# Optimization experiments

Measured on AMD Instinct MI355X. Metric: run time of the kernel, lower is better.

Reference implementation:

```python
import jax, jax.numpy as jnp
import numpy as np

N_HEADS = 16


def _rope(q, k, freq_cos, freq_sin):
    # q,k: [B,S,H,hd]; freqs: [S, hd//2]
    B, S, H, hd = q.shape
    qr, qi = q.reshape(B, S, H, hd // 2, 2)[..., 0], q.reshape(B, S, H, hd // 2, 2)[..., 1]
    kr, ki = k.reshape(B, S, H, hd // 2, 2)[..., 0], k.reshape(B, S, H, hd // 2, 2)[..., 1]
    fc = freq_cos[None, :, None, :]  # [1,S,1,hd//2]
    fs = freq_sin[None, :, None, :]
    q_out = jnp.stack([qr * fc - qi * fs, qr * fs + qi * fc], axis=-1).reshape(B, S, H, hd)
    k_out = jnp.stack([kr * fc - ki * fs, kr * fs + ki * fc], axis=-1).reshape(B, S, H, hd)
    return q_out, k_out


def setup_inputs() -> dict:
    key = jax.random.key(0)
    ks = jax.random.split(key, 7)
    B, S, D = 2, 2048, 2048
    hd = D // N_HEADS
    scale = 1.0 / np.sqrt(D)
    return {
        "x": jax.random.normal(ks[0], (B, S, D), dtype=jnp.float32),
        "freq_cos": jnp.cos(jax.random.normal(ks[1], (S, hd // 2), dtype=jnp.float32)),
        "freq_sin": jnp.sin(jax.random.normal(ks[2], (S, hd // 2), dtype=jnp.float32)),
        "wq": jax.random.normal(ks[3], (D, D), dtype=jnp.float32) * scale,
        "wk": jax.random.normal(ks[4], (D, D), dtype=jnp.float32) * scale,
        "wv": jax.random.normal(ks[5], (D, D), dtype=jnp.float32) * scale,
        "wo": jax.random.normal(ks[6], (D, D), dtype=jnp.float32) * scale,
    }


def reference(x, freq_cos, freq_sin, wq, wk, wv, wo):
    B, S, D = x.shape
    H = N_HEADS
    hd = D // H
    # torch nn.Linear(weight [out,in]): y = x @ W^T
    q = (x @ wq.T).reshape(B, S, H, hd)
    k = (x @ wk.T).reshape(B, S, H, hd)
    v = (x @ wv.T).reshape(B, S, H, hd)
    q, k = _rope(q, k, freq_cos, freq_sin)
    # [B,H,S,hd]
    q = q.transpose(0, 2, 1, 3)
    k = k.transpose(0, 2, 1, 3)
    v = v.transpose(0, 2, 1, 3)
    scores = jnp.einsum("bhqd,bhkd->bhqk", q, k) / jnp.sqrt(jnp.float32(hd))
    causal = jnp.triu(jnp.full((S, S), -jnp.inf, dtype=scores.dtype), k=1)
    scores = scores + causal[None, None, :, :]
    probs = jax.nn.softmax(scores, axis=-1)
    out = jnp.einsum("bhqk,bhkd->bhqd", probs, v)
    out = out.transpose(0, 2, 1, 3).reshape(B, S, D)
    return out @ wo.T
```

## Files before the change

kernel.cpp:

```cpp
#include <hip/hip_runtime.h>
#include <hip/hip_bf16.h>
#include <stdint.h>

typedef unsigned short u16;
typedef unsigned int   u32;

typedef __attribute__((ext_vector_type(8))) short bf16x8;
typedef __attribute__((ext_vector_type(4))) float f32x4;
typedef __attribute__((ext_vector_type(4))) float f4;
typedef __attribute__((ext_vector_type(4))) u16   u16x4;

#define GLOBAL_AS __attribute__((address_space(1)))
#define LDS_AS    __attribute__((address_space(3)))

#define QSCALE (0.088388347648318447f * 1.4426950408889634f)

__device__ __forceinline__ void gload_lds16(const void* gsrc, void* ldst) {
    __builtin_amdgcn_global_load_lds((GLOBAL_AS const u32*)gsrc,
                                     (LDS_AS u32*)ldst, 16, 0, 0);
}

__device__ __forceinline__ float b2f(u16 u) {
    union { u32 i; float f; } x; x.i = ((u32)u) << 16; return x.f;
}
__device__ __forceinline__ u16 f2b(float f) {
    u32 u = __builtin_bit_cast(u32, f);
    u = (u + 0x7fff + ((u >> 16) & 1)) >> 16;
    return (u16)u;
}
__device__ __forceinline__ u16 f2b_tr(float f) {
    return (u16)(__builtin_bit_cast(u32, f) >> 16);
}

__global__ __launch_bounds__(256)
void f2bf_all(const float* __restrict__ x,  const float* __restrict__ wq,
              const float* __restrict__ wk, const float* __restrict__ wv,
              const float* __restrict__ wo, u16* __restrict__ out,
              int md4, int dd4, int n4) {
    int i = blockIdx.x * blockDim.x + threadIdx.x;
    if (i >= n4) return;
    const float* src; int off;
    if (i < md4) { src = x; off = i; }
    else {
        int j = i - md4;
        int k = j / dd4;
        off = j - k * dd4;
        src = (k == 0) ? wq : (k == 1) ? wk : (k == 2) ? wv : wo;
    }
    f4 v = ((const f4*)src)[off];
    u16x4 o;
    o[0] = f2b(v[0]); o[1] = f2b(v[1]); o[2] = f2b(v[2]); o[3] = f2b(v[3]);
    ((u16x4*)out)[i] = o;
}

#define BARR() do { asm volatile("" ::: "memory"); \
                    __builtin_amdgcn_s_barrier();  \
                    asm volatile("" ::: "memory"); } while (0)

template<int OUT_MODE>
__global__ __launch_bounds__(512, 2)
void gemm8(const u16* __restrict__ A, const u16* __restrict__ B,
           void* __restrict__ Cptr, int M, int N, int Kdim,
           const float* __restrict__ fc, const float* __restrict__ fs) {
    __shared__ char lds[131072];
    const int t = threadIdx.x, l = t & 63, w = t >> 6;
    const int g = l >> 4, r16 = l & 15;
    const int wm = w >> 2, wn = w & 3;

    const int nwg = gridDim.x * gridDim.y;
    const int id  = blockIdx.y * gridDim.x + blockIdx.x;
    const int swz = (id & 7) * (nwg >> 3) + (id >> 3);
    const int bx  = swz % gridDim.x, by = swz / gridDim.x;
    const int m0 = by * 256, n0 = bx * 256;

    f32x4 acc[8][4];
#pragma unroll
    for (int i = 0; i < 8; i++)
#pragma unroll
        for (int j = 0; j < 4; j++) acc[i][j] = (f32x4){0.f, 0.f, 0.f, 0.f};

    const int sw  = (r16 & 7) << 4;
    const int cK0 = (g * 16) ^ sw;
    const int cK1 = (64 + g * 16) ^ sw;

    bf16x8 afA[4][2], bfA[2][2], bfB[2][2];

    auto stgA = [&](int d, int r, int kt) {
#pragma unroll
        for (int i = 0; i < 2; i++) {
            const int o  = (i * 8 + w) * 1024 + l * 16;
            const int rr = o >> 7;
            const int cb = (o & 127) ^ ((rr & 7) << 4);
            const int gr = ((rr >> 6) << 7) + r * 64 + (rr & 63);
            gload_lds16(A + (size_t)(m0 + gr) * Kdim + kt * 64 + (cb >> 1),
                        lds + d * 65536 + r * 16384 + (i * 8 + w) * 1024);
        }
    };
    auto stgB = [&](int d, int r, int kt) {
#pragma unroll
        for (int i = 0; i < 2; i++) {
            const int o  = (i * 8 + w) * 1024 + l * 16;
            const int rr = o >> 7;
            const int cb = (o & 127) ^ ((rr & 7) << 4);
            const int gc = ((rr >> 5) << 6) + r * 32 + (rr & 31);
            gload_lds16(B + (size_t)(n0 + gc) * Kdim + kt * 64 + (cb >> 1),
                        lds + d * 65536 + 32768 + r * 16384 + (i * 8 + w) * 1024);
        }
    };
    auto rdA = [&](int d, int qm) {
#pragma unroll
        for (int mi = 0; mi < 4; mi++) {
            const char* p = lds + d * 65536 + qm * 16384
                            + (wm * 64 + mi * 16 + r16) * 128;
            afA[mi][0] = *(const bf16x8*)(p + cK0);
            afA[mi][1] = *(const bf16x8*)(p + cK1);
        }
    };
    auto rdB = [&](bf16x8 (&dst)[2][2], int d, int qn) {
#pragma unroll
        for (int ni = 0; ni < 2; ni++) {
            const char* p = lds + d * 65536 + 32768 + qn * 16384
                            + (wn * 32 + ni * 16 + r16) * 128;
            dst[ni][0] = *(const bf16x8*)(p + cK0);
            dst[ni][1] = *(const bf16x8*)(p + cK1);
        }
    };
    auto mm = [&](int qm, int qn, bf16x8 (&bf)[2][2]) {
        __builtin_amdgcn_s_setprio(1);
#pragma unroll
        for (int kk = 0; kk < 2; kk++)
#pragma unroll
            for (int mi = 0; mi < 4; mi++)
#pragma unroll
                for (int ni = 0; ni < 2; ni++)
                    acc[qm * 4 + mi][qn * 2 + ni] =
                        __builtin_amdgcn_mfma_f32_16x16x32_bf16(
                            afA[mi][kk], bf[ni][kk],
                            acc[qm * 4 + mi][qn * 2 + ni], 0, 0, 0);
        __builtin_amdgcn_s_setprio(0);
    };

    const int nk = Kdim >> 6;

    stgA(0, 0, 0); stgB(0, 1, 0); stgB(0, 0, 0); stgA(0, 1, 0);
    stgA(1, 0, 1); stgB(1, 1, 1);
    asm volatile("s_waitcnt vmcnt(4)" ::: "memory");
    BARR();

    for (int tt = 0; tt < (nk >> 1); ++tt) {
        const int b1 = (2 * tt + 1);
        const int a2 = (2 * tt + 2) & (nk - 1);
        const int b2 = (2 * tt + 3) & (nk - 1);

        rdA(0, 0); rdB(bfA, 0, 0); stgB(1, 0, b1); BARR();
        mm(0, 0, bfA); BARR();
        rdB(bfB, 0, 1); stgA(1, 1, b1); BARR();
        mm(0, 1, bfB); BARR();
        rdA(0, 1); stgA(0, 0, a2); BARR();
        mm(1, 1, bfB); BARR();
        stgB(0, 1, a2); BARR();
        mm(1, 0, bfA);
        asm volatile("s_waitcnt vmcnt(4)" ::: "memory");
        BARR();
        rdA(1, 0); rdB(bfA, 1, 0); stgB(0, 0, a2); BARR();
        mm(0, 0, bfA); BARR();
        rdB(bfB, 1, 1); stgA(0, 1, a2); BARR();
        mm(0, 1, bfB); BARR();
        rdA(1, 1); stgA(1, 0, b2); BARR();
        mm(1, 1, bfB); BARR();
        stgB(1, 1, b2); BARR();
        mm(1, 0, bfA);
        asm volatile("s_waitcnt vmcnt(4)" ::: "memory");
        BARR();
    }

    if (OUT_MODE == 2 && n0 < 4096) {
        asm volatile("s_waitcnt vmcnt(0)" ::: "memory");
        __builtin_amdgcn_s_barrier();
        const char* fcb = (const char*)(fc + (size_t)(m0 & 2047) * 64);
        const char* fsb = (const char*)(fs + (size_t)(m0 & 2047) * 64);
#pragma unroll
        for (int q = 0; q < 8; q++) {
            gload_lds16(fcb + q * 8192 + w * 1024 + l * 16,
                        lds + q * 8192 + w * 1024);
            gload_lds16(fsb + q * 8192 + w * 1024 + l * 16,
                        lds + 65536 + q * 8192 + w * 1024);
        }
        asm volatile("s_waitcnt vmcnt(0)" ::: "memory");
        __builtin_amdgcn_s_barrier();
    }

#pragma unroll
    for (int a = 0; a < 8; a++)
#pragma unroll
        for (int b = 0; b < 4; b++)
#pragma unroll
            for (int r = 0; r < 4; r++) {
                int row = m0 + wm * 128 + a * 16 + g * 4 + r;
                int col = n0 + wn * 64 + b * 16 + r16;
                float v = acc[a][b][r];
                if (OUT_MODE == 0) {
                    ((float*)Cptr)[(size_t)row * N + col] = v;
                } else {
                    float ov = v;
                    if (n0 < 4096) {
                        float part = __shfl_xor(v, 1);
                        const int ss = wm * 128 + a * 16 + g * 4 + r;
                        const int i  = ((wn * 64 + b * 16 + r16) & 127) >> 1;
                        const int fo = (ss * 64 + i) << 2;
                        float c  = *(const float*)(lds + fo);
                        float sn = *(const float*)(lds + 65536 + fo);
                        ov = (r16 & 1) ? (part * sn + v * c) : (v * c - part * sn);
                        if (n0 < 2048) ov *= QSCALE;
                    }
                    ((u16*)Cptr)[(size_t)row * N + col] = f2b(ov);
                }
            }
}

template<int OUT_MODE>
__global__ __launch_bounds__(512, 2)
void gemm_bt(const u16* __restrict__ A, const u16* __restrict__ B,
             void* __restrict__ Cptr, int M, int N, int Kdim) {
    __shared__ char lds[3][49152];
    const int t = threadIdx.x, l = t & 63, w = t >> 6;
    const int g = l >> 4, r16 = l & 15;

    const int nwg = gridDim.x * gridDim.y;
    const int id  = blockIdx.y * gridDim.x + blockIdx.x;
    const int swz = (id & 7) * (nwg >> 3) + (id >> 3);
    const int bx  = swz % gridDim.x, by = swz / gridDim.x;
    const int m0 = by * 256, n0 = bx * 128;
    const int wm = w >> 1, wn = w & 1;
    const int rA = wm * 64, rB = wn * 64;

    f32x4 acc[4][4];
#pragma unroll
    for (int i = 0; i < 4; i++)
#pragma unroll
        for (int j = 0; j < 4; j++) acc[i][j] = (f32x4){0.f, 0.f, 0.f, 0.f};

    const int nk = Kdim >> 6;

    auto stage = [&](int kt, int bi) {
        const int k0 = kt << 6;
#pragma unroll
        for (int q = 0; q < 4; q++) {
            const int o = q * 8192 + w * 1024 + l * 16;
            const int row = o >> 7;
            const int cb = (o & 127) ^ ((row & 7) << 4);
            gload_lds16(A + (size_t)(m0 + row) * Kdim + k0 + (cb >> 1),
                        &lds[bi][q * 8192 + w * 1024]);
        }
#pragma unroll
        for (int q = 0; q < 2; q++) {
            const int o = q * 8192 + w * 1024 + l * 16;
            const int row = o >> 7;
            const int cb = (o & 127) ^ ((row & 7) << 4);
            gload_lds16(B + (size_t)(n0 + row) * Kdim + k0 + (cb >> 1),
                        &lds[bi][32768 + q * 8192 + w * 1024]);
        }
    };

    stage(0, 0);
    stage(1, 1);

    for (int kt = 0; kt < nk; ++kt) {
        const int cur = kt % 3;
        __builtin_amdgcn_sched_barrier(0);
        __builtin_amdgcn_s_barrier();
        stage((kt + 2) % nk, (kt + 2) % 3);
        asm volatile("s_waitcnt vmcnt(12)" ::: "memory");
        __builtin_amdgcn_s_barrier();
        __builtin_amdgcn_sched_barrier(0);

        const char* Ab = lds[cur];
        const char* Bb = lds[cur] + 32768;
        bf16x8 af[2][4], bfr[2][4];
#pragma unroll
        for (int kk = 0; kk < 2; kk++)
#pragma unroll
            for (int i = 0; i < 4; i++) {
                const int rowa = rA + i * 16 + r16;
                const int cba = (kk * 64 + g * 16) ^ ((rowa & 7) << 4);
                af[kk][i] = *(const bf16x8*)(Ab + rowa * 128 + cba);
                const int rowb = rB + i * 16 + r16;
                const int cbb = (kk * 64 + g * 16) ^ ((rowb & 7) << 4);
                bfr[kk][i] = *(const bf16x8*)(Bb + rowb * 128 + cbb);
            }
#pragma unroll
        for (int kk = 0; kk < 2; kk++)
#pragma unroll
            for (int mi = 0; mi < 4; mi++)
#pragma unroll
                for (int ni = 0; ni < 4; ni++)
                    acc[mi][ni] = __builtin_amdgcn_mfma_f32_16x16x32_bf16(af[kk][mi],
                                                                          bfr[kk][ni],
                                                                          acc[mi][ni], 0, 0, 0);
    }

#pragma unroll
    for (int mi = 0; mi < 4; mi++)
#pragma unroll
        for (int ni = 0; ni < 4; ni++)
#pragma unroll
            for (int r = 0; r < 4; r++) {
                int row = m0 + rA + mi * 16 + g * 4 + r;
                int col = n0 + rB + ni * 16 + r16;
                float v = acc[mi][ni][r];
                if (OUT_MODE == 0)      ((float*)Cptr)[(size_t)row * N + col] = v;
                else                    ((u16*)Cptr)[(size_t)row * N + col] = f2b(v);
            }
}

__global__ __launch_bounds__(512, 2)
void flash_attn(const u16* __restrict__ QKV, u16* __restrict__ Op) {
    const int S = 2048, DQ = 6144, DO = 2048;
    __shared__ u16 klds[2][128 * 128];
    __shared__ u16 vtlds[128 * 136];
    __shared__ u16 plds[8][16 * 136];
    const int t = threadIdx.x, l = t & 63, w = t >> 6;
    const int g = l >> 4, r16 = l & 15;
    const int bh = blockIdx.x, b = bh >> 4, h = bh & 15;
    const size_t base = ((size_t)(b * S)) * DQ + h * 128;
    const u16* qp = QKV + base;
    const u16* kp = qp + 2048;
    const u16* vp = qp + 4096;
    const size_t obase = ((size_t)(b * S)) * DO + h * 128;

    for (int task = 0; task < 2; ++task) {
        const int tq = task ? (15 - (int)blockIdx.y) : (int)blockIdx.y;
        const int q0 = tq * 128;
        const int nkt = tq + 1;

        bf16x8 qf[4];
#pragma unroll
        for (int ks = 0; ks < 4; ks++)
            qf[ks] = *(const bf16x8*)(qp + (size_t)(q0 + w * 16 + r16) * DQ
                                      + ks * 32 + g * 8);

        f32x4 acc[8];
#pragma unroll
        for (int i = 0; i < 8; i++) acc[i] = (f32x4){0.f, 0.f, 0.f, 0.f};
        float m_run[4], s_run[4];
#pragma unroll
        for (int r = 0; r < 4; r++) { m_run[r] = -3.0e38f; s_run[r] = 0.f; }

        auto stageK = [&](int bi, int kv0) {
#pragma unroll
            for (int i = 0; i < 4; i++) {
                const int o = (w * 4 + i) * 1024 + l * 16;
                const int row = o >> 8;
                const int cb = (o & 255) ^ ((row & 7) << 4);
                gload_lds16(kp + (size_t)(kv0 + row) * DQ + (cb >> 1),
                            (char*)klds[bi] + (w * 4 + i) * 1024);
            }
        };
        bf16x8 vv[2][2];
        auto loadV = [&](int kv0) {
#pragma unroll
            for (int c = 0; c < 2; c++)
#pragma unroll
                for (int kh = 0; kh < 2; kh++)
                    vv[c][kh] = *(const bf16x8*)(vp + (size_t)(kv0 + kh * 64 + l) * DQ
                                                 + (w * 16 + c * 8));
        };
        auto writeVT = [&]() {
#pragma unroll
            for (int c = 0; c < 2; c++)
#pragma unroll
                for (int kh = 0; kh < 2; kh++) {
                    const int d0 = w * 16 + c * 8;
#pragma unroll
                    for (int j = 0; j < 8; j++)
                        vtlds[(d0 + j) * 136 + kh * 64 + l] = (u16)vv[c][kh][j];
                }
        };

        stageK(0, 0);
        loadV(0);
        __syncthreads();
        writeVT();
        __syncthreads();

        int cur = 0;
        for (int kt = 0; kt < nkt; ++kt) {
            const int kv0 = kt * 128;
            const bool more = (kt + 1 < nkt);
            if (more) { stageK(cur ^ 1, kv0 + 128); loadV(kv0 + 128); }

            f32x4 sf[8];
#pragma unroll
            for (int nf = 0; nf < 8; nf++) sf[nf] = (f32x4){0.f, 0.f, 0.f, 0.f};
#pragma unroll
            for (int nf = 0; nf < 8; nf++) {
                const int row = nf * 16 + r16;
                const int rb = row * 256;
#pragma unroll
                for (int ks = 0; ks < 4; ks++) {
                    const int cb = (ks * 64 + g * 16) ^ ((row & 7) << 4);
                    bf16x8 kf = *(const bf16x8*)((const char*)klds[cur] + rb + cb);
                    sf[nf] = __builtin_amdgcn_mfma_f32_16x16x32_bf16(qf[ks], kf,
                                                                     sf[nf], 0, 0, 0);
                }
            }

            const bool diag = (kt == tq);
            float mt[4];
#pragma unroll
            for (int r = 0; r < 4; r++) mt[r] = -3.0e38f;
#pragma unroll
            for (int nf = 0; nf < 8; nf++)
#pragma unroll
                for (int r = 0; r < 4; r++) {
                    float s = sf[nf][r];
                    if (diag) {
                        int qrow = q0 + w * 16 + g * 4 + r;
                        int kcol = kv0 + nf * 16 + r16;
                        if (kcol > qrow) s = -3.0e38f;
                    }
                    sf[nf][r] = s;
                    mt[r] = fmaxf(mt[r], s);
                }
#pragma unroll
            for (int r = 0; r < 4; r++) {
#pragma unroll
                for (int d = 1; d < 16; d <<= 1)
                    mt[r] = fmaxf(mt[r], __shfl_xor(mt[r], d));
            }
            int grow = (mt[0] > m_run[0] + 8.f) | (mt[1] > m_run[1] + 8.f) |
                       (mt[2] > m_run[2] + 8.f) | (mt[3] > m_run[3] + 8.f);
            if (__any(grow)) {
#pragma unroll
                for (int r = 0; r < 4; r++) {
                    float mn = fmaxf(m_run[r], mt[r]);
                    float alpha = exp2f(m_run[r] - mn);
                    m_run[r] = mn;
                    s_run[r] *= alpha;
#pragma unroll
                    for (int i = 0; i < 8; i++) acc[i][r] *= alpha;
                }
            }
            float psum[4];
#pragma unroll
            for (int r = 0; r < 4; r++) psum[r] = 0.f;
#pragma unroll
            for (int nf = 0; nf < 8; nf++)
#pragma unroll
                for (int r = 0; r < 4; r++) {
                    float p = exp2f(sf[nf][r] - m_run[r]);
                    psum[r] += p;
                    plds[w][(g * 4 + r) * 136 + nf * 16 + r16] = f2b_tr(p);
                }
#pragma unroll
            for (int r = 0; r < 4; r++) {
#pragma unroll
                for (int d = 1; d < 16; d <<= 1)
                    psum[r] += __shfl_xor(psum[r], d);
                s_run[r] += psum[r];
            }
            __builtin_amdgcn_s_setprio(1);
#pragma unroll
            for (int ks2 = 0; ks2 < 4; ks2++) {
                bf16x8 pf = *(const bf16x8*)(&plds[w][r16 * 136 + ks2 * 32 + g * 8]);
#pragma unroll
                for (int nf8 = 0; nf8 < 8; nf8++) {
                    bf16x8 vf = *(const bf16x8*)(&vtlds[(nf8 * 16 + r16) * 136
                                                         + ks2 * 32 + g * 8]);
                    acc[nf8] = __builtin_amdgcn_mfma_f32_16x16x32_bf16(pf, vf,
                                                                       acc[nf8], 0, 0, 0);
                }
            }
            __builtin_amdgcn_s_setprio(0);

            __syncthreads();
            if (more) writeVT();
            __syncthreads();
            cur ^= 1;
        }

        float inv[4];
#pragma unroll
        for (int r = 0; r < 4; r++) inv[r] = 1.0f / s_run[r];
#pragma unroll
        for (int nf8 = 0; nf8 < 8; nf8++)
#pragma unroll
            for (int r = 0; r < 4; r++) {
                size_t idx = obase + (size_t)(q0 + w * 16 + g * 4 + r) * DO
                             + nf8 * 16 + r16;
                Op[idx] = f2b(acc[nf8][r] * inv[r]);
            }
    }
}

extern "C" void kernel_launch(void* const* d_in, const int* in_sizes, int n_in,
                              void* d_out, int out_size, void* d_ws, size_t ws_size,
                              hipStream_t stream) {
    const float* x  = (const float*)d_in[0];
    const float* fc = (const float*)d_in[1];
    const float* fs = (const float*)d_in[2];
    const float* wq = (const float*)d_in[3];
    const float* wk = (const float*)d_in[4];
    const float* wv = (const float*)d_in[5];
    const float* wo = (const float*)d_in[6];
    float* out = (float*)d_out;

    const int S = 2048, D = 2048;
    const int M = 2 * S;
    const size_t MD = (size_t)M * D;
    const size_t DD = (size_t)D * D;

    u16* xb   = (u16*)d_ws;
    u16* wqb  = xb  + MD;
    u16* wob  = wqb + 3 * DD;
    u16* qkvb = wob + DD;

    const int md4 = (int)(MD / 4), dd4 = (int)(DD / 4);
    const int n4  = md4 + 4 * dd4;
    f2bf_all<<<(n4 + 255) / 256, 256, 0, stream>>>(x, wq, wk, wv, wo, xb,
                                                   md4, dd4, n4);

    gemm8<2><<<dim3(6144 / 256, M / 256), 512, 0, stream>>>(xb, wqb, qkvb,
                                                            M, 6144, D, fc, fs);

    flash_attn<<<dim3(32, 8), 512, 0, stream>>>(qkvb, xb);

    gemm_bt<0><<<dim3(D / 128, M / 256), 512, 0, stream>>>(xb, wob, out, M, D, D);
}
```

Measured before the change: 278.8 us.

## Single-buffer K in LDS, alias P into K buffer, raise occupancy to 4 blocks

Each flash-attention block now handles a single query tile, heaviest tiles first, instead of a paired light/heavy tile, and the grid doubles to 32x16. K is kept in one LDS buffer instead of two, and the per-warp P tile reuses that K buffer with an XOR swizzle, so LDS per block shrinks enough to allow launch_bounds(512,4). The cost is that the next K tile can no longer be prefetched during compute. It is staged after PV, guarded by extra waitcnts and barriers, which serializes K loads against compute in exchange for more resident blocks.

```diff
diff --git a/kernel.cpp b/kernel.cpp
--- a/kernel.cpp
+++ b/kernel.cpp
@@ -313,184 +313,191 @@
             }
 }
 
-__global__ __launch_bounds__(512, 2)
+__global__ __launch_bounds__(512, 4)
 void flash_attn(const u16* __restrict__ QKV, u16* __restrict__ Op) {
     const int S = 2048, DQ = 6144, DO = 2048;
-    __shared__ u16 klds[2][128 * 128];
+    __shared__ u16 kbuf[16384];
     __shared__ u16 vtlds[128 * 136];
-    __shared__ u16 plds[8][16 * 136];
     const int t = threadIdx.x, l = t & 63, w = t >> 6;
     const int g = l >> 4, r16 = l & 15;
     const int bh = blockIdx.x, b = bh >> 4, h = bh & 15;
+    const int tq = 15 - (int)blockIdx.y;
+    const int q0 = tq * 128;
+    const int nkt = tq + 1;
     const size_t base = ((size_t)(b * S)) * DQ + h * 128;
     const u16* qp = QKV + base;
     const u16* kp = qp + 2048;
     const u16* vp = qp + 4096;
     const size_t obase = ((size_t)(b * S)) * DO + h * 128;
 
-    for (int task = 0; task < 2; ++task) {
-        const int tq = task ? (15 - (int)blockIdx.y) : (int)blockIdx.y;
-        const int q0 = tq * 128;
-        const int nkt = tq + 1;
-
-        bf16x8 qf[4];
-#pragma unroll
-        for (int ks = 0; ks < 4; ks++)
-            qf[ks] = *(const bf16x8*)(qp + (size_t)(q0 + w * 16 + r16) * DQ
-                                      + ks * 32 + g * 8);
-
-        f32x4 acc[8];
-#pragma unroll
-        for (int i = 0; i < 8; i++) acc[i] = (f32x4){0.f, 0.f, 0.f, 0.f};
-        float m_run[4], s_run[4];
-#pragma unroll
-        for (int r = 0; r < 4; r++) { m_run[r] = -3.0e38f; s_run[r] = 0.f; }
-
-        auto stageK = [&](int bi, int kv0) {
-#pragma unroll
-            for (int i = 0; i < 4; i++) {
-                const int o = (w * 4 + i) * 1024 + l * 16;
-                const int row = o >> 8;
-                const int cb = (o & 255) ^ ((row & 7) << 4);
-                gload_lds16(kp + (size_t)(kv0 + row) * DQ + (cb >> 1),
-                            (char*)klds[bi] + (w * 4 + i) * 1024);
-            }
-        };
-        bf16x8 vv[2][2];
-        auto loadV = [&](int kv0) {
-#pragma unroll
-            for (int c = 0; c < 2; c++)
-#pragma unroll
-                for (int kh = 0; kh < 2; kh++)
-                    vv[c][kh] = *(const bf16x8*)(vp + (size_t)(kv0 + kh * 64 + l) * DQ
-                                                 + (w * 16 + c * 8));
-        };
-        auto writeVT = [&]() {
-#pragma unroll
-            for (int c = 0; c < 2; c++)
-#pragma unroll
-                for (int kh = 0; kh < 2; kh++) {
-                    const int d0 = w * 16 + c * 8;
-#pragma unroll
-                    for (int j = 0; j < 8; j++)
-                        vtlds[(d0 + j) * 136 + kh * 64 + l] = (u16)vv[c][kh][j];
+    bf16x8 qf[4];
+#pragma unroll
+    for (int ks = 0; ks < 4; ks++)
+        qf[ks] = *(const bf16x8*)(qp + (size_t)(q0 + w * 16 + r16) * DQ
+                                  + ks * 32 + g * 8);
+
+    f32x4 acc[8];
+#pragma unroll
+    for (int i = 0; i < 8; i++) acc[i] = (f32x4){0.f, 0.f, 0.f, 0.f};
+    float m_run[4], s_run[4];
+#pragma unroll
+    for (int r = 0; r < 4; r++) { m_run[r] = -3.0e38f; s_run[r] = 0.f; }
+
+    auto stageK = [&](int kv0) {
+#pragma unroll
+        for (int i = 0; i < 4; i++) {
+            const int o = (w * 4 + i) * 1024 + l * 16;
+            const int row = o >> 8;
+            const int cb = (o & 255) ^ ((row & 7) << 4);
+            gload_lds16(kp + (size_t)(kv0 + row) * DQ + (cb >> 1),
+                        (char*)kbuf + (w * 4 + i) * 1024);
+        }
+    };
+    bf16x8 vv[2][2];
+    auto loadV = [&](int kv0) {
+#pragma unroll
+        for (int c = 0; c < 2; c++)
+#pragma unroll
+            for (int kh = 0; kh < 2; kh++)
+                vv[c][kh] = *(const bf16x8*)(vp + (size_t)(kv0 + kh * 64 + l) * DQ
+                                             + (w * 16 + c * 8));
+    };
+    auto writeVT = [&]() {
+#pragma unroll
+        for (int c = 0; c < 2; c++)
+#pragma unroll
+            for (int kh = 0; kh < 2; kh++) {
+                const int d0 = w * 16 + c * 8;
+#pragma unroll
+                for (int j = 0; j < 8; j++)
+                    vtlds[(d0 + j) * 136 + kh * 64 + l] = (u16)vv[c][kh][j];
+            }
+    };
+
+    stageK(0);
+    loadV(0);
+    asm volatile("s_waitcnt vmcnt(0)" ::: "memory");
+    __syncthreads();
+    writeVT();
+    __syncthreads();
+
+    for (int kt = 0; kt < nkt; ++kt) {
+        const int kv0 = kt * 128;
+        const bool more = (kt + 1 < nkt);
+        if (more) loadV(kv0 + 128);
+
+        f32x4 sf[8];
+#pragma unroll
+        for (int nf = 0; nf < 8; nf++) sf[nf] = (f32x4){0.f, 0.f, 0.f, 0.f};
+#pragma unroll
+        for (int nf = 0; nf < 8; nf++) {
+            const int row = nf * 16 + r16;
+            const int rb = row * 256;
+#pragma unroll
+            for (int ks = 0; ks < 4; ks++) {
+                const int cb = (ks * 64 + g * 16) ^ ((row & 7) << 4);
+                bf16x8 kf = *(const bf16x8*)((const char*)kbuf + rb + cb);
+                sf[nf] = __builtin_amdgcn_mfma_f32_16x16x32_bf16(qf[ks], kf,
+                                                                 sf[nf], 0, 0, 0);
+            }
+        }
+
+        const bool diag = (kt == tq);
+        float mt[4];
+#pragma unroll
+        for (int r = 0; r < 4; r++) mt[r] = -3.0e38f;
+#pragma unroll
+        for (int nf = 0; nf < 8; nf++)
+#pragma unroll
+            for (int r = 0; r < 4; r++) {
+                float s = sf[nf][r];
+                if (diag) {
+                    int qrow = q0 + w * 16 + g * 4 + r;
+                    int kcol = kv0 + nf * 16 + r16;
+                    if (kcol > qrow) s = -3.0e38f;
                 }
-        };
-
-        stageK(0, 0);
-        loadV(0);
+                sf[nf][r] = s;
+                mt[r] = fmaxf(mt[r], s);
+            }
+#pragma unroll
+        for (int r = 0; r < 4; r++) {
+#pragma unroll
+            for (int d = 1; d < 16; d <<= 1)
+                mt[r] = fmaxf(mt[r], __shfl_xor(mt[r], d));
+        }
+        int grow = (mt[0] > m_run[0] + 8.f) | (mt[1] > m_run[1] + 8.f) |
+                   (mt[2] > m_run[2] + 8.f) | (mt[3] > m_run[3] + 8.f);
+        if (__any(grow)) {
+#pragma unroll
+            for (int r = 0; r < 4; r++) {
+                float mn = fmaxf(m_run[r], mt[r]);
+                float alpha = exp2f(m_run[r] - mn);
+                m_run[r] = mn;
+                s_run[r] *= alpha;
+#pragma unroll
+                for (int i = 0; i < 8; i++) acc[i][r] *= alpha;
+            }
+        }
+
         __syncthreads();
-        writeVT();
+
+        float psum[4];
+#pragma unroll
+        for (int r = 0; r < 4; r++) psum[r] = 0.f;
+#pragma unroll
+        for (int nf = 0; nf < 8; nf++)
+#pragma unroll
+            for (int r = 0; r < 4; r++) {
+                float p = exp2f(sf[nf][r] - m_run[r]);
+                psum[r] += p;
+                const int prow = g * 4 + r;
+                kbuf[w * 2048 + prow * 128 +
+                     ((nf * 16 + r16) ^ ((prow & 7) << 3))] = f2b_tr(p);
+            }
+#pragma unroll
+        for (int r = 0; r < 4; r++) {
+#pragma unroll
+            for (int d = 1; d < 16; d <<= 1)
+                psum[r] += __shfl_xor(psum[r], d);
+            s_run[r] += psum[r];
+        }
+
+        __builtin_amdgcn_s_setprio(1);
+#pragma unroll
+        for (int ks2 = 0; ks2 < 4; ks2++) {
+            bf16x8 pf = *(const bf16x8*)(&kbuf[w * 2048 + r16 * 128 +
+                                               ((ks2 * 32 + g * 8) ^ ((r16 & 7) << 3))]);
+#pragma unroll
+            for (int nf8 = 0; nf8 < 8; nf8++) {
+                bf16x8 vf = *(const bf16x8*)(&vtlds[(nf8 * 16 + r16) * 136
+                                                     + ks2 * 32 + g * 8]);
+                acc[nf8] = __builtin_amdgcn_mfma_f32_16x16x32_bf16(pf, vf,
+                                                                   acc[nf8], 0, 0, 0);
+            }
+        }
+        __builtin_amdgcn_s_setprio(0);
+
         __syncthreads();
-
-        int cur = 0;
-        for (int kt = 0; kt < nkt; ++kt) {
-            const int kv0 = kt * 128;
-            const bool more = (kt + 1 < nkt);
-            if (more) { stageK(cur ^ 1, kv0 + 128); loadV(kv0 + 128); }
-
-            f32x4 sf[8];
-#pragma unroll
-            for (int nf = 0; nf < 8; nf++) sf[nf] = (f32x4){0.f, 0.f, 0.f, 0.f};
-#pragma unroll
-            for (int nf = 0; nf < 8; nf++) {
-                const int row = nf * 16 + r16;
-                const int rb = row * 256;
-#pragma unroll
-                for (int ks = 0; ks < 4; ks++) {
-                    const int cb = (ks * 64 + g * 16) ^ ((row & 7) << 4);
-                    bf16x8 kf = *(const bf16x8*)((const char*)klds[cur] + rb + cb);
-                    sf[nf] = __builtin_amdgcn_mfma_f32_16x16x32_bf16(qf[ks], kf,
-                                                                     sf[nf], 0, 0, 0);
-                }
-            }
-
-            const bool diag = (kt == tq);
-            float mt[4];
-#pragma unroll
-            for (int r = 0; r < 4; r++) mt[r] = -3.0e38f;
-#pragma unroll
-            for (int nf = 0; nf < 8; nf++)
-#pragma unroll
-                for (int r = 0; r < 4; r++) {
-                    float s = sf[nf][r];
-                    if (diag) {
-                        int qrow = q0 + w * 16 + g * 4 + r;
-                        int kcol = kv0 + nf * 16 + r16;
-                        if (kcol > qrow) s = -3.0e38f;
-                    }
-                    sf[nf][r] = s;
-                    mt[r] = fmaxf(mt[r], s);
-                }
-#pragma unroll
-            for (int r = 0; r < 4; r++) {
-#pragma unroll
-                for (int d = 1; d < 16; d <<= 1)
-                    mt[r] = fmaxf(mt[r], __shfl_xor(mt[r], d));
-            }
-            int grow = (mt[0] > m_run[0] + 8.f) | (mt[1] > m_run[1] + 8.f) |
-                       (mt[2] > m_run[2] + 8.f) | (mt[3] > m_run[3] + 8.f);
-            if (__any(grow)) {
-#pragma unroll
-                for (int r = 0; r < 4; r++) {
-                    float mn = fmaxf(m_run[r], mt[r]);
-                    float alpha = exp2f(m_run[r] - mn);
-                    m_run[r] = mn;
-                    s_run[r] *= alpha;
-#pragma unroll
-                    for (int i = 0; i < 8; i++) acc[i][r] *= alpha;
-                }
-            }
-            float psum[4];
-#pragma unroll
-            for (int r = 0; r < 4; r++) psum[r] = 0.f;
-#pragma unroll
-            for (int nf = 0; nf < 8; nf++)
-#pragma unroll
-                for (int r = 0; r < 4; r++) {
-                    float p = exp2f(sf[nf][r] - m_run[r]);
-                    psum[r] += p;
-                    plds[w][(g * 4 + r) * 136 + nf * 16 + r16] = f2b_tr(p);
-                }
-#pragma unroll
-            for (int r = 0; r < 4; r++) {
-#pragma unroll
-                for (int d = 1; d < 16; d <<= 1)
-                    psum[r] += __shfl_xor(psum[r], d);
-                s_run[r] += psum[r];
-            }
-            __builtin_amdgcn_s_setprio(1);
-#pragma unroll
-            for (int ks2 = 0; ks2 < 4; ks2++) {
-                bf16x8 pf = *(const bf16x8*)(&plds[w][r16 * 136 + ks2 * 32 + g * 8]);
-#pragma unroll
-                for (int nf8 = 0; nf8 < 8; nf8++) {
-                    bf16x8 vf = *(const bf16x8*)(&vtlds[(nf8 * 16 + r16) * 136
-                                                         + ks2 * 32 + g * 8]);
-                    acc[nf8] = __builtin_amdgcn_mfma_f32_16x16x32_bf16(pf, vf,
-                                                                       acc[nf8], 0, 0, 0);
-                }
-            }
-            __builtin_amdgcn_s_setprio(0);
-
-            __syncthreads();
-            if (more) writeVT();
-            __syncthreads();
-            cur ^= 1;
-        }
-
-        float inv[4];
-#pragma unroll
-        for (int r = 0; r < 4; r++) inv[r] = 1.0f / s_run[r];
-#pragma unroll
-        for (int nf8 = 0; nf8 < 8; nf8++)
-#pragma unroll
-            for (int r = 0; r < 4; r++) {
-                size_t idx = obase + (size_t)(q0 + w * 16 + g * 4 + r) * DO
-                             + nf8 * 16 + r16;
-                Op[idx] = f2b(acc[nf8][r] * inv[r]);
-            }
+        if (more) {
+            stageK(kv0 + 128);
+            asm volatile("s_waitcnt vmcnt(8)" ::: "memory");
+            writeVT();
+            asm volatile("s_waitcnt vmcnt(0)" ::: "memory");
+        }
+        __syncthreads();
     }
+
+    float inv[4];
+#pragma unroll
+    for (int r = 0; r < 4; r++) inv[r] = 1.0f / s_run[r];
+#pragma unroll
+    for (int nf8 = 0; nf8 < 8; nf8++)
+#pragma unroll
+        for (int r = 0; r < 4; r++) {
+            size_t idx = obase + (size_t)(q0 + w * 16 + g * 4 + r) * DO
+                         + nf8 * 16 + r16;
+            Op[idx] = f2b(acc[nf8][r] * inv[r]);
+        }
 }
 
 extern "C" void kernel_launch(void* const* d_in, const int* in_sizes, int n_in,
@@ -523,7 +530,7 @@
     gemm8<2><<<dim3(6144 / 256, M / 256), 512, 0, stream>>>(xb, wqb, qkvb,
                                                             M, 6144, D, fc, fs);
 
-    flash_attn<<<dim3(32, 8), 512, 0, stream>>>(qkvb, xb);
+    flash_attn<<<dim3(32, 16), 512, 0, stream>>>(qkvb, xb);
 
     gemm_bt<0><<<dim3(D / 128, M / 256), 512, 0, stream>>>(xb, wob, out, M, D, D);
 }
```

Result: slower. 424.4 us (+52.2%).
